# Optimization experiments

Hardware: AMD Instinct MI355X
Metric: run time of the kernel (lower is better)

The kernel has to match this reference:

```python
import jax, jax.numpy as jnp
import numpy as np

D_MODEL = 128
N_HEADS = 8
N_POINTS = 8
MAX_RES = 10.0


def setup_inputs() -> dict:
    key = jax.random.key(0)
    ks = jax.random.split(key, 12)
    B, C, H, W = 4, D_MODEL, 128, 128
    nh, P = N_HEADS, N_POINTS
    inp = {
        'nbr_fea': jax.random.normal(ks[0], (B, C, H, W), jnp.float32),
        'ext_fea': jax.random.normal(ks[1], (B, C, H, W), jnp.float32),
        'flow': jax.random.normal(ks[2], (B, 2, H, W), jnp.float32) * 2.0,
        'W_off': jax.random.normal(ks[3], (C, nh * P * 2), jnp.float32) * 0.02,
        'b_off': jax.random.normal(ks[4], (nh * P * 2,), jnp.float32) * 0.02,
        'W_attn': jax.random.normal(ks[5], (C, nh * P), jnp.float32) * 0.02,
        'b_attn': jnp.zeros((nh * P,), jnp.float32),
        'W_val': jax.random.normal(ks[6], (C, C), jnp.float32) * (1.0 / np.sqrt(C)),
        'b_val': jnp.zeros((C,), jnp.float32),
        'W_out': jax.random.normal(ks[7], (C, C), jnp.float32) * (1.0 / np.sqrt(C)),
        'b_out': jnp.zeros((C,), jnp.float32),
    }
    return inp


def _bilinear_gather(value, loc, H, W):
    # value: (B, nh, HW, dh)  loc: (B, nh, Q, P, 2) normalized to [0,1]
    # grid_sample semantics: align_corners=False, zero padding
    B, nh, HW, dh = value.shape
    Q, P = loc.shape[2], loc.shape[3]
    x = loc[..., 0] * W - 0.5  # (B,nh,Q,P) pixel coords
    y = loc[..., 1] * H - 0.5
    x0 = jnp.floor(x)
    y0 = jnp.floor(y)
    wx = x - x0
    wy = y - y0
    out = jnp.zeros((B, nh, Q * P, dh), value.dtype)
    for dx, dy, wgt in ((0, 0, (1 - wx) * (1 - wy)), (1, 0, wx * (1 - wy)),
                        (0, 1, (1 - wx) * wy), (1, 1, wx * wy)):
        xi = x0 + dx
        yi = y0 + dy
        valid = (xi >= 0) & (xi < W) & (yi >= 0) & (yi < H)
        xi_c = jnp.clip(xi, 0, W - 1).astype(jnp.int32)
        yi_c = jnp.clip(yi, 0, H - 1).astype(jnp.int32)
        idx = (yi_c * W + xi_c).reshape(B, nh, Q * P, 1)
        g = jnp.take_along_axis(value, idx, axis=2)  # (B,nh,QP,dh)
        w_eff = (wgt * valid.astype(value.dtype)).reshape(B, nh, Q * P, 1)
        out = out + g * w_eff
    return out.reshape(B, nh, Q, P, dh)


def reference(nbr_fea, ext_fea, flow, W_off, b_off, W_attn, b_attn, W_val, b_val, W_out, b_out):
    B, C, H, W = nbr_fea.shape
    nh, P = N_HEADS, N_POINTS
    dh = C // nh
    Q = H * W
    # normalized reference points (pixel centers / extent)
    ys = (jnp.arange(H, dtype=jnp.float32) + 0.5) / H
    xs = (jnp.arange(W, dtype=jnp.float32) + 0.5) / W
    yy, xx = jnp.meshgrid(ys, xs, indexing='ij')
    ref = jnp.stack([xx, yy], -1).reshape(Q, 2)  # (Q,2)

    ext = ext_fea.transpose(0, 2, 3, 1).reshape(B, Q, C)
    # flow-guided sampling offsets (pixels), residue bounded by tanh
    off = MAX_RES * jnp.tanh(ext @ W_off + b_off)
    off = off.reshape(B, Q, nh, P, 2)
    flow_q = flow.transpose(0, 2, 3, 1).reshape(B, Q, 1, 1, 2)
    norm = jnp.array([W, H], jnp.float32)
    loc = ref[None, :, None, None, :] + (flow_q + off) / norm  # (B,Q,nh,P,2)

    attn = jax.nn.softmax((ext @ W_attn + b_attn).reshape(B, Q, nh, P), axis=-1)

    val = (nbr_fea.transpose(0, 2, 3, 1).reshape(B, Q, C) @ W_val + b_val)
    val = val.reshape(B, Q, nh, dh).transpose(0, 2, 1, 3)  # (B,nh,HW,dh)

    sampled = _bilinear_gather(val, loc.transpose(0, 2, 1, 3, 4), H, W)  # (B,nh,Q,P,dh)
    agg = jnp.einsum('bnqpd,bqnp->bqnd', sampled, attn).reshape(B, Q, C)
    out = agg @ W_out + b_out  # (B,Q,C)
    return out.reshape(B, H, W, C).transpose(0, 3, 1, 2)
```

## Files before the change

kernel.cpp:

```cpp
#include <hip/hip_runtime.h>
#include <math.h>

namespace {
constexpr int B   = 4;
constexpr int C   = 128;
constexpr int H   = 128;
constexpr int W   = 128;
constexpr int HWn = H * W;
constexpr int NH  = 8;
constexpr int KC  = 16;
}

using short8 = __attribute__((ext_vector_type(8))) short;
using f32x4  = __attribute__((ext_vector_type(4))) float;

__device__ __forceinline__ float fast_tanh(float x) {
  float e = __expf(2.f * x);
  return 1.f - 2.f / (e + 1.f);
}
__device__ __forceinline__ unsigned f2bf(float f) {
  unsigned u = __float_as_uint(f);
  return (u + 0x7FFFu + ((u >> 16) & 1u)) >> 16;
}
__device__ __forceinline__ unsigned pack2bf(float a, float b) {
  return f2bf(a) | (f2bf(b) << 16);
}

__global__ __launch_bounds__(256) void prep_weights_kernel(
    const float* __restrict__ Woff, const float* __restrict__ Wattn,
    const float* __restrict__ Wval,
    unsigned short* __restrict__ wcat_t, unsigned short* __restrict__ wval_t) {
  int row = blockIdx.x * 256 + threadIdx.x;
  if (row >= 320) return;
  const float* src; int ldn; int col; unsigned short* dst;
  if (row < 192) {
    if (row < 128) { src = Woff; ldn = 128; col = row; }
    else           { src = Wattn; ldn = 64; col = row - 128; }
    dst = wcat_t + row * 128;
  } else {
    src = Wval; ldn = 128; col = row - 192; dst = wval_t + (row - 192) * 128;
  }
  for (int k0 = 0; k0 < 128; k0 += 8) {
    unsigned pk[4];
#pragma unroll
    for (int j = 0; j < 4; ++j)
      pk[j] = pack2bf(src[(k0 + 2 * j) * ldn + col],
                      src[(k0 + 2 * j + 1) * ldn + col]);
    *(uint4*)(dst + k0) = make_uint4(pk[0], pk[1], pk[2], pk[3]);
  }
}

__global__ __launch_bounds__(256) void gemm_kernel(
    const float* __restrict__ nbr, const float* __restrict__ ext,
    const unsigned short* __restrict__ wval_t,
    const float* __restrict__ bv,
    const unsigned short* __restrict__ wcat_t,
    const float* __restrict__ boff, const float* __restrict__ battn,
    unsigned short* __restrict__ val, float* __restrict__ proj) {
  __shared__ unsigned short a_s[64 * 152];
  __shared__ unsigned short b_s[192 * 40];
  const int t    = threadIdx.x;
  const int grp  = blockIdx.x >> 10;
  const int id   = blockIdx.x & 1023;
  const int b    = id >> 8;
  const int q0   = (id & 255) * 64;
  const int wv   = t >> 6;
  const int lane = t & 63;
  const int li   = lane & 15, quad = lane >> 4;

  const float* Ab = (grp ? ext : nbr) + (size_t)b * C * HWn + q0;
#pragma unroll
  for (int it = 0; it < 4; ++it) {
    int idx = t + 256 * it;
    int kp  = idx >> 4;
    int q4  = (idx & 15) * 4;
    float4 fa = *(const float4*)(Ab + (size_t)(2 * kp) * HWn + q4);
    float4 fb = *(const float4*)(Ab + (size_t)(2 * kp + 1) * HWn + q4);
    const float* pa = &fa.x; const float* pb = &fb.x;
#pragma unroll
    for (int j = 0; j < 4; ++j)
      *(unsigned*)&a_s[(q4 + j) * 152 + 2 * kp] = pack2bf(pa[j], pb[j]);
  }

  if (grp == 0) {
    f32x4 acc[8];
#pragma unroll
    for (int n = 0; n < 8; ++n) acc[n] = (f32x4){0.f, 0.f, 0.f, 0.f};

    for (int ck = 0; ck < 4; ++ck) {
      __syncthreads();
#pragma unroll
      for (int it = 0; it < 2; ++it) {
        int idx = t + 256 * it;
        int n = idx >> 2, seg = idx & 3;
        *(uint4*)&b_s[n * 40 + seg * 8] =
            *(const uint4*)(wval_t + n * 128 + ck * 32 + seg * 8);
      }
      __syncthreads();
      short8 af = *(const short8*)&a_s[(16 * wv + li) * 152 + ck * 32 + quad * 8];
#pragma unroll
      for (int n = 0; n < 8; ++n) {
        short8 bfr = *(const short8*)&b_s[(16 * n + li) * 40 + quad * 8];
        acc[n] = __builtin_amdgcn_mfma_f32_16x16x32_bf16(af, bfr, acc[n], 0, 0, 0);
      }
    }

    __syncthreads();
#pragma unroll
    for (int n = 0; n < 8; ++n) {
      float bias = bv[16 * n + li];
#pragma unroll
      for (int reg = 0; reg < 4; ++reg) {
        int q = 16 * wv + 4 * quad + reg;
        a_s[q * 152 + 16 * n + li] = (unsigned short)f2bf(acc[n][reg] + bias);
      }
    }
    __syncthreads();
    {
      const int qi = t & 63, r = t >> 6;
      uint4 v0 = *(const uint4*)&a_s[qi * 152 + 32 * r];
      uint4 v1 = *(const uint4*)&a_s[qi * 152 + 32 * r + 8];
      uint4 v2 = *(const uint4*)&a_s[qi * 152 + 32 * r + 16];
      uint4 v3 = *(const uint4*)&a_s[qi * 152 + 32 * r + 24];
      unsigned short* d0 = val + ((size_t)(b * NH + 2 * r) * HWn + q0 + qi) * 16;
      unsigned short* d1 = val + ((size_t)(b * NH + 2 * r + 1) * HWn + q0 + qi) * 16;
      *(uint4*)d0 = v0; *(uint4*)(d0 + 8) = v1;
      *(uint4*)d1 = v2; *(uint4*)(d1 + 8) = v3;
    }
  } else {
    f32x4 acc[12];
#pragma unroll
    for (int n = 0; n < 12; ++n) acc[n] = (f32x4){0.f, 0.f, 0.f, 0.f};

    for (int ck = 0; ck < 4; ++ck) {
      __syncthreads();
#pragma unroll
      for (int it = 0; it < 3; ++it) {
        int idx = t + 256 * it;
        int n = idx >> 2, seg = idx & 3;
        *(uint4*)&b_s[n * 40 + seg * 8] =
            *(const uint4*)(wcat_t + n * 128 + ck * 32 + seg * 8);
      }
      __syncthreads();
      short8 af = *(const short8*)&a_s[(16 * wv + li) * 152 + ck * 32 + quad * 8];
#pragma unroll
      for (int n = 0; n < 12; ++n) {
        short8 bfr = *(const short8*)&b_s[(16 * n + li) * 40 + quad * 8];
        acc[n] = __builtin_amdgcn_mfma_f32_16x16x32_bf16(af, bfr, acc[n], 0, 0, 0);
      }
    }

#pragma unroll
    for (int n = 0; n < 12; ++n) {
      int col = 16 * n + li;
      float bias = (col < 128) ? boff[col] : battn[col - 128];
#pragma unroll
      for (int reg = 0; reg < 4; ++reg) {
        int q = 16 * wv + 4 * quad + reg;
        proj[(size_t)(b * HWn + q0 + q) * 192 + col] = acc[n][reg] + bias;
      }
    }
  }
}

__global__ __launch_bounds__(256) void gather_out_kernel(
    const float* __restrict__ flow, const float* __restrict__ proj,
    const unsigned short* __restrict__ val,
    const float* __restrict__ Wout, const float* __restrict__ bout,
    float* __restrict__ out) {
  __shared__ float agg_s[C * 64];
  __shared__ float w_s[KC * 128];
  const int t  = threadIdx.x;
  const int qi = t & 63;
  const int r  = t >> 6;

  const int blk  = blockIdx.x;
  const int lin  = (blk & 7) * 128 + (blk >> 3);
  const int b    = lin >> 8;
  const int tile = lin & 255;
  const int x0   = (tile & 7) * 16;
  const int y0   = (tile >> 3) * 4;
  const int x    = x0 + (qi & 15);
  const int y    = y0 + (qi >> 4);

  const float* pp = proj + (size_t)(b * HWn + y * W + x) * 192;
  float offa[32];
  float atta[16];
#pragma unroll
  for (int j4 = 0; j4 < 8; ++j4) {
    float4 v = *(const float4*)(pp + 32 * r + 4 * j4);
    offa[4 * j4 + 0] = 10.f * fast_tanh(v.x);
    offa[4 * j4 + 1] = 10.f * fast_tanh(v.y);
    offa[4 * j4 + 2] = 10.f * fast_tanh(v.z);
    offa[4 * j4 + 3] = 10.f * fast_tanh(v.w);
  }
#pragma unroll
  for (int j4 = 0; j4 < 4; ++j4) {
    float4 v = *(const float4*)(pp + 128 + 16 * r + 4 * j4);
    atta[4 * j4 + 0] = v.x; atta[4 * j4 + 1] = v.y;
    atta[4 * j4 + 2] = v.z; atta[4 * j4 + 3] = v.w;
  }
#pragma unroll
  for (int u = 0; u < 2; ++u) {
    float* a = atta + 8 * u;
    float m = a[0];
#pragma unroll
    for (int p = 1; p < 8; ++p) m = fmaxf(m, a[p]);
    float s = 0.f;
#pragma unroll
    for (int p = 0; p < 8; ++p) { float ev = __expf(a[p] - m); a[p] = ev; s += ev; }
    float inv = 1.f / s;
#pragma unroll
    for (int p = 0; p < 8; ++p) a[p] *= inv;
  }

  const float xb = (float)x + flow[(size_t)b * 2 * HWn + y * W + x];
  const float yb = (float)y + flow[((size_t)b * 2 + 1) * HWn + y * W + x];

  float agg[32];
#pragma unroll
  for (int j = 0; j < 32; ++j) agg[j] = 0.f;
  const unsigned short* valb = val + (size_t)b * NH * HWn * 16;

#pragma unroll
  for (int u = 0; u < 2; ++u) {
    const unsigned short* valh = valb + (size_t)(2 * r + u) * HWn * 16;
    float* aggh = agg + 16 * u;
#pragma unroll
    for (int p = 0; p < 8; ++p) {
      float sx = xb + offa[u * 16 + 2 * p];
      float sy = yb + offa[u * 16 + 2 * p + 1];
      float x0f = floorf(sx), y0f = floorf(sy);
      float wx = sx - x0f, wy = sy - y0f;
      int ix0 = (int)x0f, iy0 = (int)y0f;
      int ix1 = ix0 + 1,  iy1 = iy0 + 1;
      float aw  = atta[u * 8 + p];
      float w00 = aw * (1.f - wx) * (1.f - wy);
      float w10 = aw * wx * (1.f - wy);
      float w01 = aw * (1.f - wx) * wy;
      float w11 = aw * wx * wy;
      if ((unsigned)ix0 >= (unsigned)W) { w00 = 0.f; w01 = 0.f; }
      if ((unsigned)ix1 >= (unsigned)W) { w10 = 0.f; w11 = 0.f; }
      if ((unsigned)iy0 >= (unsigned)H) { w00 = 0.f; w10 = 0.f; }
      if ((unsigned)iy1 >= (unsigned)H) { w01 = 0.f; w11 = 0.f; }
      int x0c = min(max(ix0, 0), W - 1);
      int x1c = min(max(ix1, 0), W - 1);
      int y0c = min(max(iy0, 0), H - 1);
      int y1c = min(max(iy1, 0), H - 1);
      const unsigned short* c00 = valh + (size_t)(y0c * W + x0c) * 16;
      const unsigned short* c10 = valh + (size_t)(y0c * W + x1c) * 16;
      const unsigned short* c01 = valh + (size_t)(y1c * W + x0c) * 16;
      const unsigned short* c11 = valh + (size_t)(y1c * W + x1c) * 16;
#pragma unroll
      for (int cn = 0; cn < 4; ++cn) {
        const unsigned short* cp = (cn == 0) ? c00 : (cn == 1) ? c10
                                  : (cn == 2) ? c01 : c11;
        float wgt = (cn == 0) ? w00 : (cn == 1) ? w10 : (cn == 2) ? w01 : w11;
        uint4 ga = ((const uint4*)cp)[0];
        uint4 gb = ((const uint4*)cp)[1];
        unsigned gs[8] = {ga.x, ga.y, ga.z, ga.w, gb.x, gb.y, gb.z, gb.w};
#pragma unroll
        for (int i = 0; i < 8; ++i) {
          float lo = __uint_as_float(gs[i] << 16);
          float hi = __uint_as_float(gs[i] & 0xFFFF0000u);
          aggh[2 * i]     += wgt * lo;
          aggh[2 * i + 1] += wgt * hi;
        }
      }
    }
  }

#pragma unroll
  for (int j = 0; j < 32; ++j) agg_s[(32 * r + j) * 64 + qi] = agg[j];

  float acc[32];
#pragma unroll
  for (int j = 0; j < 32; ++j) acc[j] = bout[32 * r + j];

  for (int ck = 0; ck < C / KC; ++ck) {
    const int k0 = ck * KC;
#pragma unroll
    for (int i = 0; i < 2; ++i) {
      int idx = t + 256 * i;
      int k = idx >> 5, col = (idx & 31) * 4;
      *(float4*)&w_s[k * 128 + col] =
          *(const float4*)(Wout + (size_t)(k0 + k) * 128 + col);
    }
    __syncthreads();
#pragma unroll
    for (int k = 0; k < KC; ++k) {
      float a = agg_s[(k0 + k) * 64 + qi];
      const float4* wp = (const float4*)&w_s[k * 128 + 32 * r];
#pragma unroll
      for (int j4 = 0; j4 < 8; ++j4) {
        float4 w = wp[j4];
        acc[4 * j4 + 0] += a * w.x; acc[4 * j4 + 1] += a * w.y;
        acc[4 * j4 + 2] += a * w.z; acc[4 * j4 + 3] += a * w.w;
      }
    }
    __syncthreads();
  }

  float* ob = out + (size_t)b * C * HWn + y * W + x;
#pragma unroll
  for (int j = 0; j < 32; ++j)
    ob[(size_t)(32 * r + j) * HWn] = acc[j];
}

extern "C" void kernel_launch(void* const* d_in, const int* in_sizes, int n_in,
                              void* d_out, int out_size, void* d_ws, size_t ws_size,
                              hipStream_t stream) {
  const float* nbr   = (const float*)d_in[0];
  const float* extf  = (const float*)d_in[1];
  const float* flow  = (const float*)d_in[2];
  const float* Woff  = (const float*)d_in[3];
  const float* boff  = (const float*)d_in[4];
  const float* Wattn = (const float*)d_in[5];
  const float* battn = (const float*)d_in[6];
  const float* Wval  = (const float*)d_in[7];
  const float* bval  = (const float*)d_in[8];
  const float* Wout  = (const float*)d_in[9];
  const float* bout  = (const float*)d_in[10];
  float* outp = (float*)d_out;

  unsigned short* val    = (unsigned short*)d_ws;
  unsigned short* wcat_t = val + (size_t)B * NH * HWn * 16;
  unsigned short* wval_t = wcat_t + 192 * 128;
  float*          proj   = (float*)(wval_t + 128 * 128);

  prep_weights_kernel<<<dim3(2), dim3(256), 0, stream>>>(
      Woff, Wattn, Wval, wcat_t, wval_t);
  gemm_kernel<<<dim3(2048), dim3(256), 0, stream>>>(
      nbr, extf, wval_t, bval, wcat_t, boff, battn, val, proj);
  gather_out_kernel<<<dim3(1024), dim3(256), 0, stream>>>(
      flow, proj, val, Wout, bout, outp);
}
```

Baseline: 230.6 us.

## Assign one head per thread in gather kernel, halving query tile per block

Each block in the gather/output kernel now covers 32 query pixels instead of 64, and each thread handles a single head (16 channels) instead of two. The grid doubles to 2048 blocks, the shared agg buffer halves and the Wout staging chunk shrinks to 8 rows. The goal is fewer registers per thread, so occupancy rises and more independent gathers are in flight to hide memory latency. The cost is more block-level overhead, twice as many Wout chunk reloads and syncs per pixel tile, and a shorter FMA loop in the output projection.

```diff
diff --git a/kernel.cpp b/kernel.cpp
--- a/kernel.cpp
+++ b/kernel.cpp
@@ -8,7 +8,7 @@
 constexpr int W   = 128;
 constexpr int HWn = H * W;
 constexpr int NH  = 8;
-constexpr int KC  = 16;
+constexpr int KC  = 8;
 }
 
 using short8 = __attribute__((ext_vector_type(8))) short;
@@ -168,131 +168,123 @@
     const unsigned short* __restrict__ val,
     const float* __restrict__ Wout, const float* __restrict__ bout,
     float* __restrict__ out) {
-  __shared__ float agg_s[C * 64];
+  __shared__ float agg_s[C * 32];
   __shared__ float w_s[KC * 128];
   const int t  = threadIdx.x;
-  const int qi = t & 63;
-  const int r  = t >> 6;
+  const int qi = t & 31;
+  const int r  = t >> 5;
 
   const int blk  = blockIdx.x;
-  const int lin  = (blk & 7) * 128 + (blk >> 3);
-  const int b    = lin >> 8;
-  const int tile = lin & 255;
+  const int lin  = (blk & 7) * 256 + (blk >> 3);
+  const int b    = lin >> 9;
+  const int tile = lin & 511;
   const int x0   = (tile & 7) * 16;
-  const int y0   = (tile >> 3) * 4;
+  const int y0   = (tile >> 3) * 2;
   const int x    = x0 + (qi & 15);
   const int y    = y0 + (qi >> 4);
 
   const float* pp = proj + (size_t)(b * HWn + y * W + x) * 192;
-  float offa[32];
-  float atta[16];
-#pragma unroll
-  for (int j4 = 0; j4 < 8; ++j4) {
-    float4 v = *(const float4*)(pp + 32 * r + 4 * j4);
+  float offa[16];
+  float atta[8];
+#pragma unroll
+  for (int j4 = 0; j4 < 4; ++j4) {
+    float4 v = *(const float4*)(pp + 16 * r + 4 * j4);
     offa[4 * j4 + 0] = 10.f * fast_tanh(v.x);
     offa[4 * j4 + 1] = 10.f * fast_tanh(v.y);
     offa[4 * j4 + 2] = 10.f * fast_tanh(v.z);
     offa[4 * j4 + 3] = 10.f * fast_tanh(v.w);
   }
 #pragma unroll
-  for (int j4 = 0; j4 < 4; ++j4) {
-    float4 v = *(const float4*)(pp + 128 + 16 * r + 4 * j4);
+  for (int j4 = 0; j4 < 2; ++j4) {
+    float4 v = *(const float4*)(pp + 128 + 8 * r + 4 * j4);
     atta[4 * j4 + 0] = v.x; atta[4 * j4 + 1] = v.y;
     atta[4 * j4 + 2] = v.z; atta[4 * j4 + 3] = v.w;
   }
-#pragma unroll
-  for (int u = 0; u < 2; ++u) {
-    float* a = atta + 8 * u;
-    float m = a[0];
-#pragma unroll
-    for (int p = 1; p < 8; ++p) m = fmaxf(m, a[p]);
+  {
+    float m = atta[0];
+#pragma unroll
+    for (int p = 1; p < 8; ++p) m = fmaxf(m, atta[p]);
     float s = 0.f;
 #pragma unroll
-    for (int p = 0; p < 8; ++p) { float ev = __expf(a[p] - m); a[p] = ev; s += ev; }
+    for (int p = 0; p < 8; ++p) { float ev = __expf(atta[p] - m); atta[p] = ev; s += ev; }
     float inv = 1.f / s;
 #pragma unroll
-    for (int p = 0; p < 8; ++p) a[p] *= inv;
+    for (int p = 0; p < 8; ++p) atta[p] *= inv;
   }
 
   const float xb = (float)x + flow[(size_t)b * 2 * HWn + y * W + x];
   const float yb = (float)y + flow[((size_t)b * 2 + 1) * HWn + y * W + x];
 
-  float agg[32];
-#pragma unroll
-  for (int j = 0; j < 32; ++j) agg[j] = 0.f;
-  const unsigned short* valb = val + (size_t)b * NH * HWn * 16;
-
-#pragma unroll
-  for (int u = 0; u < 2; ++u) {
-    const unsigned short* valh = valb + (size_t)(2 * r + u) * HWn * 16;
-    float* aggh = agg + 16 * u;
-#pragma unroll
-    for (int p = 0; p < 8; ++p) {
-      float sx = xb + offa[u * 16 + 2 * p];
-      float sy = yb + offa[u * 16 + 2 * p + 1];
-      float x0f = floorf(sx), y0f = floorf(sy);
-      float wx = sx - x0f, wy = sy - y0f;
-      int ix0 = (int)x0f, iy0 = (int)y0f;
-      int ix1 = ix0 + 1,  iy1 = iy0 + 1;
-      float aw  = atta[u * 8 + p];
-      float w00 = aw * (1.f - wx) * (1.f - wy);
-      float w10 = aw * wx * (1.f - wy);
-      float w01 = aw * (1.f - wx) * wy;
-      float w11 = aw * wx * wy;
-      if ((unsigned)ix0 >= (unsigned)W) { w00 = 0.f; w01 = 0.f; }
-      if ((unsigned)ix1 >= (unsigned)W) { w10 = 0.f; w11 = 0.f; }
-      if ((unsigned)iy0 >= (unsigned)H) { w00 = 0.f; w10 = 0.f; }
-      if ((unsigned)iy1 >= (unsigned)H) { w01 = 0.f; w11 = 0.f; }
-      int x0c = min(max(ix0, 0), W - 1);
-      int x1c = min(max(ix1, 0), W - 1);
-      int y0c = min(max(iy0, 0), H - 1);
-      int y1c = min(max(iy1, 0), H - 1);
-      const unsigned short* c00 = valh + (size_t)(y0c * W + x0c) * 16;
-      const unsigned short* c10 = valh + (size_t)(y0c * W + x1c) * 16;
-      const unsigned short* c01 = valh + (size_t)(y1c * W + x0c) * 16;
-      const unsigned short* c11 = valh + (size_t)(y1c * W + x1c) * 16;
-#pragma unroll
-      for (int cn = 0; cn < 4; ++cn) {
-        const unsigned short* cp = (cn == 0) ? c00 : (cn == 1) ? c10
-                                  : (cn == 2) ? c01 : c11;
-        float wgt = (cn == 0) ? w00 : (cn == 1) ? w10 : (cn == 2) ? w01 : w11;
-        uint4 ga = ((const uint4*)cp)[0];
-        uint4 gb = ((const uint4*)cp)[1];
-        unsigned gs[8] = {ga.x, ga.y, ga.z, ga.w, gb.x, gb.y, gb.z, gb.w};
-#pragma unroll
-        for (int i = 0; i < 8; ++i) {
-          float lo = __uint_as_float(gs[i] << 16);
-          float hi = __uint_as_float(gs[i] & 0xFFFF0000u);
-          aggh[2 * i]     += wgt * lo;
-          aggh[2 * i + 1] += wgt * hi;
-        }
-      }
-    }
-  }
-
-#pragma unroll
-  for (int j = 0; j < 32; ++j) agg_s[(32 * r + j) * 64 + qi] = agg[j];
-
-  float acc[32];
-#pragma unroll
-  for (int j = 0; j < 32; ++j) acc[j] = bout[32 * r + j];
+  float agg[16];
+#pragma unroll
+  for (int j = 0; j < 16; ++j) agg[j] = 0.f;
+  const unsigned short* valh =
+      val + ((size_t)b * NH + r) * HWn * 16;
+
+#pragma unroll
+  for (int p = 0; p < 8; ++p) {
+    float sx = xb + offa[2 * p];
+    float sy = yb + offa[2 * p + 1];
+    float x0f = floorf(sx), y0f = floorf(sy);
+    float wx = sx - x0f, wy = sy - y0f;
+    int ix0 = (int)x0f, iy0 = (int)y0f;
+    int ix1 = ix0 + 1,  iy1 = iy0 + 1;
+    float aw  = atta[p];
+    float w00 = aw * (1.f - wx) * (1.f - wy);
+    float w10 = aw * wx * (1.f - wy);
+    float w01 = aw * (1.f - wx) * wy;
+    float w11 = aw * wx * wy;
+    if ((unsigned)ix0 >= (unsigned)W) { w00 = 0.f; w01 = 0.f; }
+    if ((unsigned)ix1 >= (unsigned)W) { w10 = 0.f; w11 = 0.f; }
+    if ((unsigned)iy0 >= (unsigned)H) { w00 = 0.f; w10 = 0.f; }
+    if ((unsigned)iy1 >= (unsigned)H) { w01 = 0.f; w11 = 0.f; }
+    int x0c = min(max(ix0, 0), W - 1);
+    int x1c = min(max(ix1, 0), W - 1);
+    int y0c = min(max(iy0, 0), H - 1);
+    int y1c = min(max(iy1, 0), H - 1);
+    const unsigned short* c00 = valh + (size_t)(y0c * W + x0c) * 16;
+    const unsigned short* c10 = valh + (size_t)(y0c * W + x1c) * 16;
+    const unsigned short* c01 = valh + (size_t)(y1c * W + x0c) * 16;
+    const unsigned short* c11 = valh + (size_t)(y1c * W + x1c) * 16;
+#pragma unroll
+    for (int cn = 0; cn < 4; ++cn) {
+      const unsigned short* cp = (cn == 0) ? c00 : (cn == 1) ? c10
+                                : (cn == 2) ? c01 : c11;
+      float wgt = (cn == 0) ? w00 : (cn == 1) ? w10 : (cn == 2) ? w01 : w11;
+      uint4 ga = ((const uint4*)cp)[0];
+      uint4 gb = ((const uint4*)cp)[1];
+      unsigned gs[8] = {ga.x, ga.y, ga.z, ga.w, gb.x, gb.y, gb.z, gb.w};
+#pragma unroll
+      for (int i = 0; i < 8; ++i) {
+        float lo = __uint_as_float(gs[i] << 16);
+        float hi = __uint_as_float(gs[i] & 0xFFFF0000u);
+        agg[2 * i]     += wgt * lo;
+        agg[2 * i + 1] += wgt * hi;
+      }
+    }
+  }
+
+#pragma unroll
+  for (int j = 0; j < 16; ++j) agg_s[(16 * r + j) * 32 + qi] = agg[j];
+
+  float acc[16];
+#pragma unroll
+  for (int j = 0; j < 16; ++j) acc[j] = bout[16 * r + j];
 
   for (int ck = 0; ck < C / KC; ++ck) {
     const int k0 = ck * KC;
-#pragma unroll
-    for (int i = 0; i < 2; ++i) {
-      int idx = t + 256 * i;
-      int k = idx >> 5, col = (idx & 31) * 4;
+    {
+      int k = t >> 5, col = (t & 31) * 4;
       *(float4*)&w_s[k * 128 + col] =
           *(const float4*)(Wout + (size_t)(k0 + k) * 128 + col);
     }
     __syncthreads();
 #pragma unroll
     for (int k = 0; k < KC; ++k) {
-      float a = agg_s[(k0 + k) * 64 + qi];
-      const float4* wp = (const float4*)&w_s[k * 128 + 32 * r];
-#pragma unroll
-      for (int j4 = 0; j4 < 8; ++j4) {
+      float a = agg_s[(k0 + k) * 32 + qi];
+      const float4* wp = (const float4*)&w_s[k * 128 + 16 * r];
+#pragma unroll
+      for (int j4 = 0; j4 < 4; ++j4) {
         float4 w = wp[j4];
         acc[4 * j4 + 0] += a * w.x; acc[4 * j4 + 1] += a * w.y;
         acc[4 * j4 + 2] += a * w.z; acc[4 * j4 + 3] += a * w.w;
@@ -303,8 +295,8 @@
 
   float* ob = out + (size_t)b * C * HWn + y * W + x;
 #pragma unroll
-  for (int j = 0; j < 32; ++j)
-    ob[(size_t)(32 * r + j) * HWn] = acc[j];
+  for (int j = 0; j < 16; ++j)
+    ob[(size_t)(16 * r + j) * HWn] = acc[j];
 }
 
 extern "C" void kernel_launch(void* const* d_in, const int* in_sizes, int n_in,
@@ -332,6 +324,6 @@
       Woff, Wattn, Wval, wcat_t, wval_t);
   gemm_kernel<<<dim3(2048), dim3(256), 0, stream>>>(
       nbr, extf, wval_t, bval, wcat_t, boff, battn, val, proj);
-  gather_out_kernel<<<dim3(1024), dim3(256), 0, stream>>>(
+  gather_out_kernel<<<dim3(2048), dim3(256), 0, stream>>>(
       flow, proj, val, Wout, bout, outp);
 }
```

Result: no change. 235.1 us (+1.9%).
